# Optimization experiments

Measured on AMD Instinct MI355X. Metric: run time of the kernel, lower is better.

## Reference

```python
import jax, jax.numpy as jnp
import numpy as np

B, L, D = 32, 2048, 64
MASK_FILL = -1.0e6  # matches torch code's -1000000.0


def setup_inputs() -> dict:
    key = jax.random.key(0)
    kq, kk, kv, kl = jax.random.split(key, 4)
    queries = jax.random.normal(kq, (B, L, D), dtype=jnp.float32)
    keys = jax.random.normal(kk, (B, L, D), dtype=jnp.float32)
    values = jax.random.normal(kv, (B, L, D), dtype=jnp.float32)
    valid_lens = jax.random.randint(kl, (B,), 1, L + 1, dtype=jnp.int64)
    return {"queries": queries, "keys": keys, "values": values,
            "valid_lens": valid_lens}


def reference(queries, keys, values, valid_lens):
    d = queries.shape[-1]
    # [B, Lq, Lk] scores
    scores = jnp.einsum('bqd,bkd->bqk', queries, keys) / jnp.sqrt(
        jnp.asarray(d, dtype=queries.dtype))
    # length mask: position k valid iff k < valid_lens[b]
    Lk = scores.shape[-1]
    mask = jnp.arange(Lk)[None, :] < valid_lens[:, None]      # [B, Lk]
    scores = jnp.where(mask[:, None, :], scores, MASK_FILL)   # broadcast over Lq
    attn = jax.nn.softmax(scores, axis=-1)
    # dropout p=0.0 -> identity
    return jnp.einsum('bqk,bkv->bqv', attn, values)
```

## Files before the change

kernel.cpp:

```cpp
#include <hip/hip_runtime.h>
#include <hip/hip_bf16.h>
#include <math.h>


#define BB 32
#define LL 2048
#define DD 64
#define QBLK 128
#define KBLK 64
#define NTICKETS (BB * (LL / QBLK))
#define GRID 384

typedef __attribute__((ext_vector_type(8))) short bf16x8;
typedef __attribute__((ext_vector_type(4))) short bf16x4;
typedef __attribute__((ext_vector_type(4))) float f32x4;

static __device__ __forceinline__ short f2bf(float f) {
    __hip_bfloat16 h = __float2bfloat16(f);
    return *reinterpret_cast<short*>(&h);
}
static __device__ __forceinline__ unsigned pk2(float a, float b) {
    return (unsigned)(unsigned short)f2bf(a) | ((unsigned)(unsigned short)f2bf(b) << 16);
}
static __device__ __forceinline__ float exp2c(float x) {
    return __builtin_amdgcn_exp2f(x);
}

static __device__ __forceinline__ f32x4 mfma16(bf16x4 a, bf16x4 b, f32x4 c) {
#if __has_builtin(__builtin_amdgcn_mfma_f32_16x16x16bf16_1k)
    return __builtin_amdgcn_mfma_f32_16x16x16bf16_1k(a, b, c, 0, 0, 0);
#else
    asm("v_mfma_f32_16x16x16_bf16 %0, %1, %2, %0" : "+v"(c) : "v"(a), "v"(b));
    return c;
#endif
}

static __device__ __forceinline__ void cp16(const char* g, char* lbase, int lane) {
#if __has_builtin(__builtin_amdgcn_global_load_lds)
    __builtin_amdgcn_global_load_lds(
        (__attribute__((address_space(1))) void*)g,
        (__attribute__((address_space(3))) void*)lbase, 16, 0, 0);
#else
    *reinterpret_cast<uint4*>(lbase + lane * 16) = *reinterpret_cast<const uint4*>(g);
#endif
}

__global__ void init_ctr_kernel(const int* __restrict__ vlen, int* __restrict__ ws) {
    int t = threadIdx.x;
    if (t == 0) ws[0] = 0;
    if (t < BB) {
        int v = vlen[t];
        int rank = 0;
        for (int j = 0; j < BB; ++j) {
            int vj = vlen[j];
            rank += (vj > v) || (vj == v && j < t);
        }
        ws[1 + rank] = t;
    }
}

__global__ __launch_bounds__(256) void convert_kv_kernel(
    const float* __restrict__ K, const float* __restrict__ V,
    unsigned short* __restrict__ kv)
{
    const int tile = blockIdx.x;
    const int tid  = threadIdx.x;
    const float*  Kt  = K + (size_t)tile * (KBLK * DD);
    const float4* Vg4 = reinterpret_cast<const float4*>(V + (size_t)tile * (KBLK * DD));
    unsigned short* img = kv + (size_t)tile * 8192;

    #pragma unroll
    for (int g = 0; g < 2; ++g) {
        int e = tid + g * 256;
        int f = e >> 6, L = e & 63;
        int t = f >> 1, ds = f & 1;
        int lq = L & 15, lg = L >> 4;
        const float4* src = reinterpret_cast<const float4*>(
            Kt + (t * 16 + lq) * DD + ds * 32 + lg * 8);
        float4 a = src[0], c = src[1];
        uint4 w;
        w.x = pk2(a.x, a.y); w.y = pk2(a.z, a.w);
        w.z = pk2(c.x, c.y); w.w = pk2(c.z, c.w);
        *reinterpret_cast<uint4*>(img + (size_t)e * 8) = w;
    }

    unsigned short* img2 = img + 4096;
    const int vd4 = (tid & 15) * 4;
    const int vkr = (tid >> 4) * 4;
    const int vt  = vkr >> 4;
    const int vlg = (vkr >> 2) & 3;
    float4 v0 = Vg4[(vkr + 0) * 16 + (tid & 15)];
    float4 v1 = Vg4[(vkr + 1) * 16 + (tid & 15)];
    float4 v2 = Vg4[(vkr + 2) * 16 + (tid & 15)];
    float4 v3 = Vg4[(vkr + 3) * 16 + (tid & 15)];
    const float* p0 = (const float*)&v0;
    const float* p1 = (const float*)&v1;
    const float* p2 = (const float*)&v2;
    const float* p3 = (const float*)&v3;
    #pragma unroll
    for (int j = 0; j < 4; ++j) {
        int col = vd4 + j;
        int n = col >> 4, lq = col & 15;
        int L = vlg * 16 + lq;
        uint2 w = make_uint2(pk2(p0[j], p1[j]), pk2(p2[j], p3[j]));
        *reinterpret_cast<uint2*>(img2 + (size_t)(n * 4 + vt) * 256 + L * 4) = w;
    }
}

__global__ __launch_bounds__(512, 1) void attn_mfma_kernel(
    const float* __restrict__ Q, const int* __restrict__ vlen,
    const unsigned short* __restrict__ kvimg,
    float* __restrict__ O, int* __restrict__ ws)
{
    __shared__ __align__(16) unsigned short Buf[3][8192];
    __shared__ int s_tile;

    int* ctr = ws;
    const int* order = ws + 1;

    const int tid  = threadIdx.x;
    const int wid  = tid >> 6;
    const int lane = tid & 63;
    const int lq   = lane & 15;
    const int lg   = lane >> 4;

    const float QSCALE = 0.125f * 1.44269504088896341f;

    for (;;) {
        __syncthreads();
        if (tid == 0) s_tile = atomicAdd(ctr, 1);
        __syncthreads();
        const int tile = s_tile;
        if (tile >= NTICKETS) break;

        const int b     = order[tile >> 4];
        const int qt    = tile & 15;
        const int qbase = qt * QBLK + wid * 16;
        const int valid = vlen[b];
        const int ntiles = (valid + KBLK - 1) / KBLK;

        const unsigned short* tbase = kvimg + (size_t)b * (32 * 8192);

        auto dma = [&](int t, int bi) {
            const char* g = (const char*)(tbase + (size_t)t * 8192)
                            + wid * 2048 + lane * 16;
            char* l = (char*)&Buf[bi][0] + wid * 2048;
            cp16(g,        l,        lane);
            cp16(g + 1024, l + 1024, lane);
        };

        bf16x8 qf[2];
        {
            const float* Qr = Q + ((size_t)b * LL + qbase + lq) * DD;
            #pragma unroll
            for (int ds_ = 0; ds_ < 2; ++ds_) {
                const float4* p4 = reinterpret_cast<const float4*>(Qr + ds_ * 32 + lg * 8);
                float4 a = p4[0], c = p4[1];
                bf16x8 f;
                f[0] = f2bf(a.x * QSCALE); f[1] = f2bf(a.y * QSCALE);
                f[2] = f2bf(a.z * QSCALE); f[3] = f2bf(a.w * QSCALE);
                f[4] = f2bf(c.x * QSCALE); f[5] = f2bf(c.y * QSCALE);
                f[6] = f2bf(c.z * QSCALE); f[7] = f2bf(c.w * QSCALE);
                qf[ds_] = f;
            }
        }

        f32x4 acc[4];
        #pragma unroll
        for (int n = 0; n < 4; ++n) acc[n] = (f32x4){0.f, 0.f, 0.f, 0.f};
        float m_ = -1e30f, l_ = 0.f;

        auto qkt = [&](int bi, f32x4* s) {
            const unsigned short* kb = &Buf[bi][0];
            __builtin_amdgcn_s_setprio(1);
            #pragma unroll
            for (int t = 0; t < 4; ++t) {
                f32x4 a = (f32x4){0.f, 0.f, 0.f, 0.f};
                #pragma unroll
                for (int ds_ = 0; ds_ < 2; ++ds_) {
                    bf16x8 kf = *reinterpret_cast<const bf16x8*>(
                        &kb[(size_t)(t * 2 + ds_) * 512 + lane * 8]);
                    a = __builtin_amdgcn_mfma_f32_16x16x32_bf16(kf, qf[ds_], a, 0, 0, 0);
                }
                s[t] = a;
            }
            __builtin_amdgcn_s_setprio(0);
        };

        auto smpv = [&](int kt, f32x4* s, int bi) {
            const bool tail = (kt == ntiles - 1) && (valid & (KBLK - 1));
            if (tail) {
                #pragma unroll
                for (int t = 0; t < 4; ++t)
                    #pragma unroll
                    for (int r = 0; r < 4; ++r) {
                        int kg = kt * KBLK + t * 16 + lg * 4 + r;
                        if (kg >= valid) s[t][r] = -1e30f;
                    }
            }
            float mx = s[0][0];
            #pragma unroll
            for (int t = 0; t < 4; ++t)
                #pragma unroll
                for (int r = 0; r < 4; ++r) mx = fmaxf(mx, s[t][r]);
            mx = fmaxf(mx, __shfl_xor(mx, 16, 64));
            mx = fmaxf(mx, __shfl_xor(mx, 32, 64));

            if (__any(mx - m_ > 8.0f)) {
                float mnew = fmaxf(m_, mx);
                float corr = exp2c(m_ - mnew);
                m_ = mnew;
                l_ *= corr;
                #pragma unroll
                for (int r = 0; r < 4; ++r) {
                    float cq = __shfl(corr, lg * 4 + r, 64);
                    #pragma unroll
                    for (int n = 0; n < 4; ++n) acc[n][r] *= cq;
                }
            }

            float ls = 0.f;
            #pragma unroll
            for (int t = 0; t < 4; ++t)
                #pragma unroll
                for (int r = 0; r < 4; ++r) {
                    float p = exp2c(s[t][r] - m_);
                    s[t][r] = p;
                    ls += p;
                }
            ls += __shfl_xor(ls, 16, 64);
            ls += __shfl_xor(ls, 32, 64);
            l_ += ls;

            const unsigned short* vb = &Buf[bi][4096];
            __builtin_amdgcn_s_setprio(1);
            #pragma unroll
            for (int t = 0; t < 4; ++t) {
                union { uint2 u; bf16x4 v; } pa;
                pa.u = make_uint2(pk2(s[t][0], s[t][1]), pk2(s[t][2], s[t][3]));
                #pragma unroll
                for (int n = 0; n < 4; ++n) {
                    union { uint2 u; bf16x4 v; } vv;
                    vv.u = *reinterpret_cast<const uint2*>(
                        &vb[(size_t)(n * 4 + t) * 256 + lane * 4]);
                    acc[n] = mfma16(pa.v, vv.v, acc[n]);
                }
            }
            __builtin_amdgcn_s_setprio(0);
        };

        int bc = 0, bn = 1, bd = 2;
        dma(0, 0);
        if (ntiles > 1) dma(1, 1);
        __syncthreads();
        f32x4 sA[4], sB[4];
        qkt(0, sA);

        int t = 0;
        for (; t + 2 <= ntiles; t += 2) {
            if (t + 2 < ntiles) dma(t + 2, bd);
            qkt(bn, sB);
            smpv(t, sA, bc);
            __syncthreads();
            { int x = bc; bc = bn; bn = bd; bd = x; }
            if (t + 3 < ntiles) dma(t + 3, bd);
            if (t + 2 < ntiles) qkt(bn, sA);
            smpv(t + 1, sB, bc);
            __syncthreads();
            { int x = bc; bc = bn; bn = bd; bd = x; }
        }
        if (t < ntiles) smpv(t, sA, bc);

        float linv[4];
        #pragma unroll
        for (int r = 0; r < 4; ++r)
            linv[r] = 1.f / __shfl(l_, lg * 4 + r, 64);
        float* Ob = O + ((size_t)b * LL + qbase) * DD;
        #pragma unroll
        for (int n = 0; n < 4; ++n) {
            #pragma unroll
            for (int r = 0; r < 4; ++r) {
                Ob[(size_t)(lg * 4 + r) * DD + n * 16 + lq] = acc[n][r] * linv[r];
            }
        }
    }
}

extern "C" void kernel_launch(void* const* d_in, const int* in_sizes, int n_in,
                              void* d_out, int out_size, void* d_ws, size_t ws_size,
                              hipStream_t stream) {
    const float* Q = (const float*)d_in[0];
    const float* K = (const float*)d_in[1];
    const float* V = (const float*)d_in[2];
    const int* vlen = (const int*)d_in[3];
    float* O = (float*)d_out;

    int* ws_i = (int*)d_ws;
    unsigned short* kvimg = (unsigned short*)((char*)d_ws + 1024);

    init_ctr_kernel<<<1, 64, 0, stream>>>(vlen, ws_i);
    convert_kv_kernel<<<BB * (LL / KBLK), 256, 0, stream>>>(K, V, kvimg);
    attn_mfma_kernel<<<GRID, 512, 0, stream>>>(Q, vlen, kvimg, O, ws_i);
}
```

Before: 68.97 us.

## Switch attention to 32x32x16 MFMA with 4-wave blocks and new KV layout

Replaces the 16x16 MFMA tiles with 32x32x16 bf16 MFMA, so each wave now owns 32 query rows and each block runs 4 waves (256 threads, two blocks per CU). The K/V image layout in the conversion kernel is rewritten to match the new fragment shapes. P fragments are rebuilt with lane-crossing shuffles, and row statistics become per-lane, which removes the per-row shuffles for the correction and normalization. Output stores are vectorized to float4. The larger MFMA shape and lower reduction overhead come at the cost of extra cross-half shuffles, higher register pressure, and a strided V read in the conversion kernel.

```diff
diff --git a/kernel.cpp b/kernel.cpp
--- a/kernel.cpp
+++ b/kernel.cpp
@@ -12,8 +12,7 @@
 #define GRID 384
 
 typedef __attribute__((ext_vector_type(8))) short bf16x8;
-typedef __attribute__((ext_vector_type(4))) short bf16x4;
-typedef __attribute__((ext_vector_type(4))) float f32x4;
+typedef __attribute__((ext_vector_type(16))) float f32x16;
 
 static __device__ __forceinline__ short f2bf(float f) {
     __hip_bfloat16 h = __float2bfloat16(f);
@@ -25,14 +24,8 @@
 static __device__ __forceinline__ float exp2c(float x) {
     return __builtin_amdgcn_exp2f(x);
 }
-
-static __device__ __forceinline__ f32x4 mfma16(bf16x4 a, bf16x4 b, f32x4 c) {
-#if __has_builtin(__builtin_amdgcn_mfma_f32_16x16x16bf16_1k)
-    return __builtin_amdgcn_mfma_f32_16x16x16bf16_1k(a, b, c, 0, 0, 0);
-#else
-    asm("v_mfma_f32_16x16x16_bf16 %0, %1, %2, %0" : "+v"(c) : "v"(a), "v"(b));
-    return c;
-#endif
+static __device__ __forceinline__ f32x16 mfma32(bf16x8 a, bf16x8 b, f32x16 c) {
+    return __builtin_amdgcn_mfma_f32_32x32x16_bf16(a, b, c, 0, 0, 0);
 }
 
 static __device__ __forceinline__ void cp16(const char* g, char* lbase, int lane) {
@@ -65,49 +58,44 @@
 {
     const int tile = blockIdx.x;
     const int tid  = threadIdx.x;
-    const float*  Kt  = K + (size_t)tile * (KBLK * DD);
-    const float4* Vg4 = reinterpret_cast<const float4*>(V + (size_t)tile * (KBLK * DD));
+    const float* Kt = K + (size_t)tile * (KBLK * DD);
+    const float* Vt = V + (size_t)tile * (KBLK * DD);
     unsigned short* img = kv + (size_t)tile * 8192;
 
     #pragma unroll
     for (int g = 0; g < 2; ++g) {
         int e = tid + g * 256;
         int f = e >> 6, L = e & 63;
-        int t = f >> 1, ds = f & 1;
-        int lq = L & 15, lg = L >> 4;
-        const float4* src = reinterpret_cast<const float4*>(
-            Kt + (t * 16 + lq) * DD + ds * 32 + lg * 8);
-        float4 a = src[0], c = src[1];
+        int kh = f >> 2, c = f & 3;
+        int krow = kh * 32 + (L & 31);
+        int dbase = 16 * c + 8 * (L >> 5);
+        const float4* src = reinterpret_cast<const float4*>(Kt + krow * DD + dbase);
+        float4 a = src[0], b = src[1];
         uint4 w;
         w.x = pk2(a.x, a.y); w.y = pk2(a.z, a.w);
-        w.z = pk2(c.x, c.y); w.w = pk2(c.z, c.w);
+        w.z = pk2(b.x, b.y); w.w = pk2(b.z, b.w);
         *reinterpret_cast<uint4*>(img + (size_t)e * 8) = w;
     }
 
     unsigned short* img2 = img + 4096;
-    const int vd4 = (tid & 15) * 4;
-    const int vkr = (tid >> 4) * 4;
-    const int vt  = vkr >> 4;
-    const int vlg = (vkr >> 2) & 3;
-    float4 v0 = Vg4[(vkr + 0) * 16 + (tid & 15)];
-    float4 v1 = Vg4[(vkr + 1) * 16 + (tid & 15)];
-    float4 v2 = Vg4[(vkr + 2) * 16 + (tid & 15)];
-    float4 v3 = Vg4[(vkr + 3) * 16 + (tid & 15)];
-    const float* p0 = (const float*)&v0;
-    const float* p1 = (const float*)&v1;
-    const float* p2 = (const float*)&v2;
-    const float* p3 = (const float*)&v3;
     #pragma unroll
-    for (int j = 0; j < 4; ++j) {
-        int col = vd4 + j;
-        int n = col >> 4, lq = col & 15;
-        int L = vlg * 16 + lq;
-        uint2 w = make_uint2(pk2(p0[j], p1[j]), pk2(p2[j], p3[j]));
-        *reinterpret_cast<uint2*>(img2 + (size_t)(n * 4 + vt) * 256 + L * 4) = w;
+    for (int g = 0; g < 2; ++g) {
+        int e = tid + g * 256;
+        int f = e >> 6, L = e & 63;
+        int n = f >> 2, c = f & 3;
+        int col = 32 * n + (L & 31);
+        int kbase = 16 * c + 8 * (L >> 5);
+        float v[8];
+        #pragma unroll
+        for (int j = 0; j < 8; ++j) v[j] = Vt[(kbase + j) * DD + col];
+        uint4 w;
+        w.x = pk2(v[0], v[1]); w.y = pk2(v[2], v[3]);
+        w.z = pk2(v[4], v[5]); w.w = pk2(v[6], v[7]);
+        *reinterpret_cast<uint4*>(img2 + (size_t)e * 8) = w;
     }
 }
 
-__global__ __launch_bounds__(512, 1) void attn_mfma_kernel(
+__global__ __launch_bounds__(256, 2) void attn_mfma_kernel(
     const float* __restrict__ Q, const int* __restrict__ vlen,
     const unsigned short* __restrict__ kvimg,
     float* __restrict__ O, int* __restrict__ ws)
@@ -121,8 +109,8 @@
     const int tid  = threadIdx.x;
     const int wid  = tid >> 6;
     const int lane = tid & 63;
-    const int lq   = lane & 15;
-    const int lg   = lane >> 4;
+    const int l31  = lane & 31;
+    const int hi   = lane >> 5;
 
     const float QSCALE = 0.125f * 1.44269504088896341f;
 
@@ -135,7 +123,7 @@
 
         const int b     = order[tile >> 4];
         const int qt    = tile & 15;
-        const int qbase = qt * QBLK + wid * 16;
+        const int qbase = qt * QBLK + wid * 32;
         const int valid = vlen[b];
         const int ntiles = (valid + KBLK - 1) / KBLK;
 
@@ -143,67 +131,70 @@
 
         auto dma = [&](int t, int bi) {
             const char* g = (const char*)(tbase + (size_t)t * 8192)
-                            + wid * 2048 + lane * 16;
-            char* l = (char*)&Buf[bi][0] + wid * 2048;
+                            + wid * 4096 + lane * 16;
+            char* l = (char*)&Buf[bi][0] + wid * 4096;
             cp16(g,        l,        lane);
             cp16(g + 1024, l + 1024, lane);
+            cp16(g + 2048, l + 2048, lane);
+            cp16(g + 3072, l + 3072, lane);
         };
 
-        bf16x8 qf[2];
+        bf16x8 qf[4];
         {
-            const float* Qr = Q + ((size_t)b * LL + qbase + lq) * DD;
-            #pragma unroll
-            for (int ds_ = 0; ds_ < 2; ++ds_) {
-                const float4* p4 = reinterpret_cast<const float4*>(Qr + ds_ * 32 + lg * 8);
-                float4 a = p4[0], c = p4[1];
+            const float* Qr = Q + ((size_t)b * LL + qbase + l31) * DD;
+            #pragma unroll
+            for (int c = 0; c < 4; ++c) {
+                const float4* p4 = reinterpret_cast<const float4*>(Qr + 16 * c + 8 * hi);
+                float4 a = p4[0], d = p4[1];
                 bf16x8 f;
                 f[0] = f2bf(a.x * QSCALE); f[1] = f2bf(a.y * QSCALE);
                 f[2] = f2bf(a.z * QSCALE); f[3] = f2bf(a.w * QSCALE);
-                f[4] = f2bf(c.x * QSCALE); f[5] = f2bf(c.y * QSCALE);
-                f[6] = f2bf(c.z * QSCALE); f[7] = f2bf(c.w * QSCALE);
-                qf[ds_] = f;
+                f[4] = f2bf(d.x * QSCALE); f[5] = f2bf(d.y * QSCALE);
+                f[6] = f2bf(d.z * QSCALE); f[7] = f2bf(d.w * QSCALE);
+                qf[c] = f;
             }
         }
 
-        f32x4 acc[4];
+        f32x16 acc[2];
         #pragma unroll
-        for (int n = 0; n < 4; ++n) acc[n] = (f32x4){0.f, 0.f, 0.f, 0.f};
+        for (int i = 0; i < 16; ++i) { acc[0][i] = 0.f; acc[1][i] = 0.f; }
         float m_ = -1e30f, l_ = 0.f;
 
-        auto qkt = [&](int bi, f32x4* s) {
+        auto qkt = [&](int bi, f32x16* s) {
             const unsigned short* kb = &Buf[bi][0];
             __builtin_amdgcn_s_setprio(1);
             #pragma unroll
-            for (int t = 0; t < 4; ++t) {
-                f32x4 a = (f32x4){0.f, 0.f, 0.f, 0.f};
-                #pragma unroll
-                for (int ds_ = 0; ds_ < 2; ++ds_) {
+            for (int kh = 0; kh < 2; ++kh) {
+                f32x16 a;
+                #pragma unroll
+                for (int i = 0; i < 16; ++i) a[i] = 0.f;
+                #pragma unroll
+                for (int c = 0; c < 4; ++c) {
                     bf16x8 kf = *reinterpret_cast<const bf16x8*>(
-                        &kb[(size_t)(t * 2 + ds_) * 512 + lane * 8]);
-                    a = __builtin_amdgcn_mfma_f32_16x16x32_bf16(kf, qf[ds_], a, 0, 0, 0);
+                        &kb[(size_t)(kh * 4 + c) * 512 + lane * 8]);
+                    a = mfma32(kf, qf[c], a);
                 }
-                s[t] = a;
+                s[kh] = a;
             }
             __builtin_amdgcn_s_setprio(0);
         };
 
-        auto smpv = [&](int kt, f32x4* s, int bi) {
+        auto smpv = [&](int kt, f32x16* s, int bi) {
             const bool tail = (kt == ntiles - 1) && (valid & (KBLK - 1));
             if (tail) {
                 #pragma unroll
-                for (int t = 0; t < 4; ++t)
+                for (int kh = 0; kh < 2; ++kh)
                     #pragma unroll
-                    for (int r = 0; r < 4; ++r) {
-                        int kg = kt * KBLK + t * 16 + lg * 4 + r;
-                        if (kg >= valid) s[t][r] = -1e30f;
+                    for (int r = 0; r < 16; ++r) {
+                        int kg = kt * KBLK + kh * 32 + (r & 3) + 8 * (r >> 2) + 4 * hi;
+                        if (kg >= valid) s[kh][r] = -1e30f;
                     }
             }
             float mx = s[0][0];
             #pragma unroll
-            for (int t = 0; t < 4; ++t)
-                #pragma unroll
-                for (int r = 0; r < 4; ++r) mx = fmaxf(mx, s[t][r]);
-            mx = fmaxf(mx, __shfl_xor(mx, 16, 64));
+            for (int r = 1; r < 16; ++r) mx = fmaxf(mx, s[0][r]);
+            #pragma unroll
+            for (int r = 0; r < 16; ++r) mx = fmaxf(mx, s[1][r]);
             mx = fmaxf(mx, __shfl_xor(mx, 32, 64));
 
             if (__any(mx - m_ > 8.0f)) {
@@ -212,38 +203,51 @@
                 m_ = mnew;
                 l_ *= corr;
                 #pragma unroll
-                for (int r = 0; r < 4; ++r) {
-                    float cq = __shfl(corr, lg * 4 + r, 64);
-                    #pragma unroll
-                    for (int n = 0; n < 4; ++n) acc[n][r] *= cq;
-                }
+                for (int i = 0; i < 16; ++i) { acc[0][i] *= corr; acc[1][i] *= corr; }
             }
 
             float ls = 0.f;
             #pragma unroll
-            for (int t = 0; t < 4; ++t)
-                #pragma unroll
-                for (int r = 0; r < 4; ++r) {
-                    float p = exp2c(s[t][r] - m_);
-                    s[t][r] = p;
+            for (int kh = 0; kh < 2; ++kh)
+                #pragma unroll
+                for (int r = 0; r < 16; ++r) {
+                    float p = exp2c(s[kh][r] - m_);
+                    s[kh][r] = p;
                     ls += p;
                 }
-            ls += __shfl_xor(ls, 16, 64);
             ls += __shfl_xor(ls, 32, 64);
             l_ += ls;
 
+            bf16x8 pf[4];
+            #pragma unroll
+            for (int c = 0; c < 4; ++c) {
+                const int T = c >> 1;
+                const int b0 = 8 * (c & 1);
+                unsigned A0 = pk2(s[T][b0 + 0], s[T][b0 + 1]);
+                unsigned A1 = pk2(s[T][b0 + 2], s[T][b0 + 3]);
+                unsigned B0 = pk2(s[T][b0 + 4], s[T][b0 + 5]);
+                unsigned B1 = pk2(s[T][b0 + 6], s[T][b0 + 7]);
+                unsigned xA0 = (unsigned)__shfl_xor((int)A0, 32, 64);
+                unsigned xA1 = (unsigned)__shfl_xor((int)A1, 32, 64);
+                unsigned xB0 = (unsigned)__shfl_xor((int)B0, 32, 64);
+                unsigned xB1 = (unsigned)__shfl_xor((int)B1, 32, 64);
+                union { uint4 u; bf16x8 v; } fr;
+                fr.u.x = hi ? xB0 : A0;
+                fr.u.y = hi ? xB1 : A1;
+                fr.u.z = hi ? B0 : xA0;
+                fr.u.w = hi ? B1 : xA1;
+                pf[c] = fr.v;
+            }
+
             const unsigned short* vb = &Buf[bi][4096];
             __builtin_amdgcn_s_setprio(1);
             #pragma unroll
-            for (int t = 0; t < 4; ++t) {
-                union { uint2 u; bf16x4 v; } pa;
-                pa.u = make_uint2(pk2(s[t][0], s[t][1]), pk2(s[t][2], s[t][3]));
-                #pragma unroll
-                for (int n = 0; n < 4; ++n) {
-                    union { uint2 u; bf16x4 v; } vv;
-                    vv.u = *reinterpret_cast<const uint2*>(
-                        &vb[(size_t)(n * 4 + t) * 256 + lane * 4]);
-                    acc[n] = mfma16(pa.v, vv.v, acc[n]);
+            for (int n = 0; n < 2; ++n) {
+                #pragma unroll
+                for (int c = 0; c < 4; ++c) {
+                    bf16x8 vf = *reinterpret_cast<const bf16x8*>(
+                        &vb[(size_t)(n * 4 + c) * 512 + lane * 8]);
+                    acc[n] = mfma32(vf, pf[c], acc[n]);
                 }
             }
             __builtin_amdgcn_s_setprio(0);
@@ -253,7 +257,7 @@
         dma(0, 0);
         if (ntiles > 1) dma(1, 1);
         __syncthreads();
-        f32x4 sA[4], sB[4];
+        f32x16 sA[2], sB[2];
         qkt(0, sA);
 
         int t = 0;
@@ -271,16 +275,18 @@
         }
         if (t < ntiles) smpv(t, sA, bc);
 
-        float linv[4];
+        float linv = 1.f / l_;
+        float* Ob = O + ((size_t)b * LL + qbase + l31) * DD;
         #pragma unroll
-        for (int r = 0; r < 4; ++r)
-            linv[r] = 1.f / __shfl(l_, lg * 4 + r, 64);
-        float* Ob = O + ((size_t)b * LL + qbase) * DD;
-        #pragma unroll
-        for (int n = 0; n < 4; ++n) {
-            #pragma unroll
-            for (int r = 0; r < 4; ++r) {
-                Ob[(size_t)(lg * 4 + r) * DD + n * 16 + lq] = acc[n][r] * linv[r];
+        for (int n = 0; n < 2; ++n) {
+            #pragma unroll
+            for (int u = 0; u < 4; ++u) {
+                float4 o;
+                o.x = acc[n][4 * u + 0] * linv;
+                o.y = acc[n][4 * u + 1] * linv;
+                o.z = acc[n][4 * u + 2] * linv;
+                o.w = acc[n][4 * u + 3] * linv;
+                *reinterpret_cast<float4*>(Ob + 32 * n + 8 * u + 4 * hi) = o;
             }
         }
     }
@@ -300,5 +306,5 @@
 
     init_ctr_kernel<<<1, 64, 0, stream>>>(vlen, ws_i);
     convert_kv_kernel<<<BB * (LL / KBLK), 256, 0, stream>>>(K, V, kvimg);
-    attn_mfma_kernel<<<GRID, 512, 0, stream>>>(Q, vlen, kvimg, O, ws_i);
-}
+    attn_mfma_kernel<<<GRID, 256, 0, stream>>>(Q, vlen, kvimg, O, ws_i);
+}
```

After: 77.64 us. 1.13x slower.
